# Performance work log

Hardware: AMD Instinct MI355X
Metric: run time of the kernel (lower is better)

Reference implementation:

```python
import jax, jax.numpy as jnp
import numpy as np

N_PED = 131072      # total pedestrians (batch)
SEG = 64            # pedestrians per segment (equal-size groups)
N_SEQ = N_PED // SEG
D_IN = 256          # enc_h_dim
D_OUT = 128         # mlp_dim


def setup_inputs() -> dict:
    key = jax.random.key(0)
    k1, k2 = jax.random.split(key, 2)
    h_states = jax.random.normal(k1, (N_PED, D_IN), dtype=jnp.float32)
    W = jax.random.normal(k2, (D_IN, D_OUT), dtype=jnp.float32) * 0.05
    b = jnp.zeros((D_OUT,), dtype=jnp.float32)
    starts = jnp.arange(N_SEQ, dtype=jnp.int64) * SEG
    seq_start_end = jnp.stack([starts, starts + SEG], axis=1)  # [N_SEQ, 2]
    return {"h_states": h_states, "W": W, "b": b, "seq_start_end": seq_start_end}


def reference(h_states, W, b, seq_start_end):
    # fc projection: (N, D_IN) -> (N, D_OUT)
    h = h_states @ W + b
    # gather each segment: equal-size groups of SEG pedestrians
    starts = seq_start_end[:, 0]                     # [G]
    idx = starts[:, None] + jnp.arange(SEG)[None, :]  # [G, S]
    seg = h[idx]                                      # [G, S, D_OUT]
    # per-segment self-attention pooling: softmax(H H^T) @ H
    scores = jnp.einsum('gsd,gtd->gst', seg, seg)     # [G, S, S]
    attn = jax.nn.softmax(scores, axis=-1)
    ctx = jnp.einsum('gst,gtd->gsd', attn, seg)       # [G, S, D_OUT]
    return ctx.reshape(-1, D_OUT)                     # [N, D_OUT]
```

## Files before the change

kernel.cpp:

```cpp
#include <hip/hip_runtime.h>
#include <stdint.h>

#define SEG 64
#define D_IN 256
#define D_OUT 128
#define NSEQ 2048

typedef __attribute__((ext_vector_type(8))) _Float16 half8;
typedef __attribute__((ext_vector_type(4))) float floatx4;

static __device__ __forceinline__ unsigned short f2h_bits(float f) {
  union { _Float16 h; unsigned short u; } v; v.h = (_Float16)f; return v.u;
}
static __device__ __forceinline__ unsigned pack2(float a, float b) {
  return (unsigned)f2h_bits(a) | ((unsigned)f2h_bits(b) << 16);
}

__global__ void prep_w_kernel(const float* __restrict__ W,
                              unsigned short* __restrict__ Wf) {
  const int idx = blockIdx.x * 256 + threadIdx.x;
  const float v = W[idx];
  const int k = idx >> 7, n = idx & 127;
  const int slot = (((n >> 4) * 8 + (k >> 5)) * 64 + ((n & 15) + 16 * ((k >> 3) & 3))) * 8 + (k & 7);
  Wf[slot] = f2h_bits(v);
}

struct SharedHT {
  union {
    unsigned short h[4][4][64][8];
    unsigned short pb[4][2][64][8];
  };
  unsigned short ht[8][2][64][8];
};
union alignas(16) SharedU {
  unsigned short a[4][8][64][8];
  SharedHT s;
};

__global__ __launch_bounds__(256, 4)
void attn_fused(const float* __restrict__ hs,
                const unsigned short* __restrict__ Wf,
                const float* __restrict__ bias,
                float* __restrict__ out)
{
  __shared__ SharedU u;

  const int g    = blockIdx.x;
  const int tid  = (int)threadIdx.x;
  const int w    = tid >> 6;
  const int lane = tid & 63;
  const int c    = lane & 15;
  const int q    = lane >> 4;

  {
    const float4* gsrc = (const float4*)(hs + (size_t)g * (SEG * D_IN));
#pragma unroll
    for (int i = 0; i < 4; ++i) {
      const int qb = i * 1024 + tid * 4;
      const float4 v0 = gsrc[qb + 0];
      const float4 v1 = gsrc[qb + 1];
      const float4 v2 = gsrc[qb + 2];
      const float4 v3 = gsrc[qb + 3];
      const int row  = i * 16 + (tid >> 4);
      const int ks   = (tid & 15) >> 1;
      const int slot = (row & 15) + ((tid & 1) << 5);
      unsigned short* d0 = &u.a[row >> 4][ks][slot][0];
      uint4 wa, wb;
      wa.x = pack2(v0.x, v0.y); wa.y = pack2(v0.z, v0.w);
      wa.z = pack2(v1.x, v1.y); wa.w = pack2(v1.z, v1.w);
      wb.x = pack2(v2.x, v2.y); wb.y = pack2(v2.z, v2.w);
      wb.z = pack2(v3.x, v3.y); wb.w = pack2(v3.z, v3.w);
      *(uint4*)d0         = wa;
      *(uint4*)(d0 + 128) = wb;
    }
  }

  const half8* WfV = (const half8*)Wf;
  const half8 wpre0 = WfV[((2 * w + 0) * 8 + 0) * 64 + lane];
  const half8 wpre1 = WfV[((2 * w + 1) * 8 + 0) * 64 + lane];

  float bv[2];
#pragma unroll
  for (int nt = 0; nt < 2; ++nt) bv[nt] = bias[(2 * w + nt) * 16 + c];
  floatx4 acc[2][4];
#pragma unroll
  for (int nt = 0; nt < 2; ++nt)
#pragma unroll
    for (int mt = 0; mt < 4; ++mt)
      acc[nt][mt] = (floatx4){bv[nt], bv[nt], bv[nt], bv[nt]};

  __syncthreads();

#pragma unroll
  for (int ks = 0; ks < 8; ++ks) {
    const half8 wf0 = ks ? WfV[((2 * w + 0) * 8 + ks) * 64 + lane] : wpre0;
    const half8 wf1 = ks ? WfV[((2 * w + 1) * 8 + ks) * 64 + lane] : wpre1;
    half8 af[4];
#pragma unroll
    for (int mt = 0; mt < 4; ++mt)
      af[mt] = *(const half8*)(&u.a[mt][ks][lane][0]);
#pragma unroll
    for (int mt = 0; mt < 4; ++mt) {
      acc[0][mt] = __builtin_amdgcn_mfma_f32_16x16x32_f16(af[mt], wf0, acc[0][mt], 0, 0, 0);
      acc[1][mt] = __builtin_amdgcn_mfma_f32_16x16x32_f16(af[mt], wf1, acc[1][mt], 0, 0, 0);
    }
  }

  __syncthreads();

#pragma unroll
  for (int nt = 0; nt < 2; ++nt) {
    const int ntg = 2 * w + nt;
#pragma unroll
    for (int mt = 0; mt < 4; ++mt) {
      unsigned short hb[4];
#pragma unroll
      for (int i = 0; i < 4; ++i) hb[i] = f2h_bits(acc[nt][mt][i]);
      const int lph = 16 * ((2 * nt + (c >> 3)) & 3);
#pragma unroll
      for (int i = 0; i < 4; ++i)
        u.s.h[mt][w][4 * q + i + lph][c & 7] = hb[i];
      const int lanep = c + 16 * ((2 * mt + (q >> 1)) & 3);
      const unsigned lo = (unsigned)hb[0] | ((unsigned)hb[1] << 16);
      const unsigned hi = (unsigned)hb[2] | ((unsigned)hb[3] << 16);
      *(uint2*)(&u.s.ht[ntg][mt >> 1][lanep][(q & 1) * 4]) = make_uint2(lo, hi);
    }
  }

  __syncthreads();

  floatx4 sacc[4];
#pragma unroll
  for (int nt = 0; nt < 4; ++nt) sacc[nt] = (floatx4){0.f, 0.f, 0.f, 0.f};
#pragma unroll
  for (int ks = 0; ks < 4; ++ks) {
    const half8 a = *(const half8*)(&u.s.h[w][ks][lane][0]);
#pragma unroll
    for (int nt = 0; nt < 4; ++nt) {
      const half8 b = *(const half8*)(&u.s.h[nt][ks][lane][0]);
      sacc[nt] = __builtin_amdgcn_mfma_f32_16x16x32_f16(a, b, sacc[nt], 0, 0, 0);
    }
  }

  float ev[4][4];
  float inv[4];
#pragma unroll
  for (int i = 0; i < 4; ++i) {
    float m = fmaxf(fmaxf(sacc[0][i], sacc[1][i]), fmaxf(sacc[2][i], sacc[3][i]));
#pragma unroll
    for (int d = 1; d < 16; d <<= 1) m = fmaxf(m, __shfl_xor(m, d, 64));
    float ssum = 0.f;
#pragma unroll
    for (int nt = 0; nt < 4; ++nt) {
      ev[i][nt] = __expf(sacc[nt][i] - m);
      ssum += ev[i][nt];
    }
#pragma unroll
    for (int d = 1; d < 16; d <<= 1) ssum += __shfl_xor(ssum, d, 64);
    inv[i] = 1.0f / ssum;
  }

  __syncthreads();

#pragma unroll
  for (int i = 0; i < 4; ++i)
#pragma unroll
    for (int nt = 0; nt < 4; ++nt)
      u.s.pb[w][nt >> 1][4 * q + i + 16 * ((2 * nt + (c >> 3)) & 3)][c & 7] =
          f2h_bits(ev[i][nt] * inv[i]);

  floatx4 cacc[8];
#pragma unroll
  for (int dt = 0; dt < 8; ++dt) cacc[dt] = (floatx4){0.f, 0.f, 0.f, 0.f};
#pragma unroll
  for (int kt = 0; kt < 2; ++kt) {
    const half8 pf = *(const half8*)(&u.s.pb[w][kt][lane][0]);
#pragma unroll
    for (int dt = 0; dt < 8; ++dt) {
      const half8 hf = *(const half8*)(&u.s.ht[dt][kt][lane][0]);
      cacc[dt] = __builtin_amdgcn_mfma_f32_16x16x32_f16(hf, pf, cacc[dt], 0, 0, 0);
    }
  }

  float* orow = out + ((size_t)g * SEG + 16 * w + c) * D_OUT + 4 * q;
#pragma unroll
  for (int dt = 0; dt < 8; ++dt)
    *(floatx4*)(orow + 16 * dt) = cacc[dt];
}

extern "C" void kernel_launch(void* const* d_in, const int* in_sizes, int n_in,
                              void* d_out, int out_size, void* d_ws, size_t ws_size,
                              hipStream_t stream) {
  const float* hs   = (const float*)d_in[0];
  const float* W    = (const float*)d_in[1];
  const float* bias = (const float*)d_in[2];
  float* out = (float*)d_out;
  unsigned short* Wf = (unsigned short*)d_ws;

  prep_w_kernel<<<128, 256, 0, stream>>>(W, Wf);
  attn_fused<<<NSEQ, 256, 0, stream>>>(hs, Wf, bias, out);
}
```

Measured before the change: 221.8 us.

## Make attention kernel persistent with register-staged prefetch of next segment

The grid shrinks from one block per segment to 512 persistent blocks, each looping over four segments. While the current segment's projection runs, the next segment's input is loaded into registers and written to a separate, no-longer-aliased shared buffer, so global-load latency overlaps with MFMA work. The cost is a larger shared footprint and heavy register use (16 float4 staging registers), and launch bounds drop to 2 blocks per CU, which lowers occupancy and may give less latency hiding than the original many-block launch.

New measurement: 222.7 us. About the same (+0.4%).

```diff
diff --git a/kernel.cpp b/kernel.cpp
--- a/kernel.cpp
+++ b/kernel.cpp
@@ -5,6 +5,7 @@
 #define D_IN 256
 #define D_OUT 128
 #define NSEQ 2048
+#define NBLK 512
 
 typedef __attribute__((ext_vector_type(8))) _Float16 half8;
 typedef __attribute__((ext_vector_type(4))) float floatx4;
@@ -32,28 +33,32 @@
   };
   unsigned short ht[8][2][64][8];
 };
-union alignas(16) SharedU {
+struct alignas(16) SharedAll {
   unsigned short a[4][8][64][8];
   SharedHT s;
 };
 
-__global__ __launch_bounds__(256, 4)
+__global__ __launch_bounds__(256, 2)
 void attn_fused(const float* __restrict__ hs,
                 const unsigned short* __restrict__ Wf,
                 const float* __restrict__ bias,
                 float* __restrict__ out)
 {
-  __shared__ SharedU u;
-
-  const int g    = blockIdx.x;
+  __shared__ SharedAll u;
+
+  const int bid  = blockIdx.x;
   const int tid  = (int)threadIdx.x;
   const int w    = tid >> 6;
   const int lane = tid & 63;
   const int c    = lane & 15;
   const int q    = lane >> 4;
 
+  const int srow  = tid >> 4;
+  const int sks   = (tid & 15) >> 1;
+  const int sslot = ((tid & 1) << 5);
+
   {
-    const float4* gsrc = (const float4*)(hs + (size_t)g * (SEG * D_IN));
+    const float4* gsrc = (const float4*)(hs + (size_t)bid * (SEG * D_IN));
 #pragma unroll
     for (int i = 0; i < 4; ++i) {
       const int qb = i * 1024 + tid * 4;
@@ -61,10 +66,8 @@
       const float4 v1 = gsrc[qb + 1];
       const float4 v2 = gsrc[qb + 2];
       const float4 v3 = gsrc[qb + 3];
-      const int row  = i * 16 + (tid >> 4);
-      const int ks   = (tid & 15) >> 1;
-      const int slot = (row & 15) + ((tid & 1) << 5);
-      unsigned short* d0 = &u.a[row >> 4][ks][slot][0];
+      const int row = i * 16 + srow;
+      unsigned short* d0 = &u.a[row >> 4][sks][(row & 15) + sslot][0];
       uint4 wa, wb;
       wa.x = pack2(v0.x, v0.y); wa.y = pack2(v0.z, v0.w);
       wa.z = pack2(v1.x, v1.y); wa.w = pack2(v1.z, v1.w);
@@ -75,117 +78,149 @@
     }
   }
 
+  float bv[2];
+#pragma unroll
+  for (int nt = 0; nt < 2; ++nt) bv[nt] = bias[(2 * w + nt) * 16 + c];
+
   const half8* WfV = (const half8*)Wf;
-  const half8 wpre0 = WfV[((2 * w + 0) * 8 + 0) * 64 + lane];
-  const half8 wpre1 = WfV[((2 * w + 1) * 8 + 0) * 64 + lane];
-
-  float bv[2];
-#pragma unroll
-  for (int nt = 0; nt < 2; ++nt) bv[nt] = bias[(2 * w + nt) * 16 + c];
-  floatx4 acc[2][4];
-#pragma unroll
-  for (int nt = 0; nt < 2; ++nt)
-#pragma unroll
-    for (int mt = 0; mt < 4; ++mt)
-      acc[nt][mt] = (floatx4){bv[nt], bv[nt], bv[nt], bv[nt]};
 
   __syncthreads();
 
-#pragma unroll
-  for (int ks = 0; ks < 8; ++ks) {
-    const half8 wf0 = ks ? WfV[((2 * w + 0) * 8 + ks) * 64 + lane] : wpre0;
-    const half8 wf1 = ks ? WfV[((2 * w + 1) * 8 + ks) * 64 + lane] : wpre1;
-    half8 af[4];
-#pragma unroll
-    for (int mt = 0; mt < 4; ++mt)
-      af[mt] = *(const half8*)(&u.a[mt][ks][lane][0]);
-#pragma unroll
-    for (int mt = 0; mt < 4; ++mt) {
-      acc[0][mt] = __builtin_amdgcn_mfma_f32_16x16x32_f16(af[mt], wf0, acc[0][mt], 0, 0, 0);
-      acc[1][mt] = __builtin_amdgcn_mfma_f32_16x16x32_f16(af[mt], wf1, acc[1][mt], 0, 0, 0);
-    }
+  for (int it = 0; it < 4; ++it) {
+    const int seg = bid + NBLK * it;
+
+    float4 st[16];
+    if (it < 3) {
+      const float4* gn = (const float4*)(hs + (size_t)(seg + NBLK) * (SEG * D_IN));
+#pragma unroll
+      for (int i = 0; i < 4; ++i)
+#pragma unroll
+        for (int k2 = 0; k2 < 4; ++k2)
+          st[4 * i + k2] = gn[i * 1024 + tid * 4 + k2];
+    }
+
+    floatx4 acc[2][4];
+#pragma unroll
+    for (int nt = 0; nt < 2; ++nt)
+#pragma unroll
+      for (int mt = 0; mt < 4; ++mt)
+        acc[nt][mt] = (floatx4){bv[nt], bv[nt], bv[nt], bv[nt]};
+
+#pragma unroll
+    for (int ks = 0; ks < 8; ++ks) {
+      const half8 wf0 = WfV[((2 * w + 0) * 8 + ks) * 64 + lane];
+      const half8 wf1 = WfV[((2 * w + 1) * 8 + ks) * 64 + lane];
+      half8 af[4];
+#pragma unroll
+      for (int mt = 0; mt < 4; ++mt)
+        af[mt] = *(const half8*)(&u.a[mt][ks][lane][0]);
+#pragma unroll
+      for (int mt = 0; mt < 4; ++mt) {
+        acc[0][mt] = __builtin_amdgcn_mfma_f32_16x16x32_f16(af[mt], wf0, acc[0][mt], 0, 0, 0);
+        acc[1][mt] = __builtin_amdgcn_mfma_f32_16x16x32_f16(af[mt], wf1, acc[1][mt], 0, 0, 0);
+      }
+    }
+
+    __syncthreads();
+
+    if (it < 3) {
+#pragma unroll
+      for (int i = 0; i < 4; ++i) {
+        const int row = i * 16 + srow;
+        unsigned short* d0 = &u.a[row >> 4][sks][(row & 15) + sslot][0];
+        uint4 wa, wb;
+        wa.x = pack2(st[4 * i + 0].x, st[4 * i + 0].y);
+        wa.y = pack2(st[4 * i + 0].z, st[4 * i + 0].w);
+        wa.z = pack2(st[4 * i + 1].x, st[4 * i + 1].y);
+        wa.w = pack2(st[4 * i + 1].z, st[4 * i + 1].w);
+        wb.x = pack2(st[4 * i + 2].x, st[4 * i + 2].y);
+        wb.y = pack2(st[4 * i + 2].z, st[4 * i + 2].w);
+        wb.z = pack2(st[4 * i + 3].x, st[4 * i + 3].y);
+        wb.w = pack2(st[4 * i + 3].z, st[4 * i + 3].w);
+        *(uint4*)d0         = wa;
+        *(uint4*)(d0 + 128) = wb;
+      }
+    }
+
+#pragma unroll
+    for (int nt = 0; nt < 2; ++nt) {
+      const int ntg = 2 * w + nt;
+#pragma unroll
+      for (int mt = 0; mt < 4; ++mt) {
+        unsigned short hb[4];
+#pragma unroll
+        for (int i = 0; i < 4; ++i) hb[i] = f2h_bits(acc[nt][mt][i]);
+        const int lph = 16 * ((2 * nt + (c >> 3)) & 3);
+#pragma unroll
+        for (int i = 0; i < 4; ++i)
+          u.s.h[mt][w][4 * q + i + lph][c & 7] = hb[i];
+        const int lanep = c + 16 * ((2 * mt + (q >> 1)) & 3);
+        const unsigned lo = (unsigned)hb[0] | ((unsigned)hb[1] << 16);
+        const unsigned hi = (unsigned)hb[2] | ((unsigned)hb[3] << 16);
+        *(uint2*)(&u.s.ht[ntg][mt >> 1][lanep][(q & 1) * 4]) = make_uint2(lo, hi);
+      }
+    }
+
+    __syncthreads();
+
+    floatx4 sacc[4];
+#pragma unroll
+    for (int nt = 0; nt < 4; ++nt) sacc[nt] = (floatx4){0.f, 0.f, 0.f, 0.f};
+#pragma unroll
+    for (int ks = 0; ks < 4; ++ks) {
+      const half8 a = *(const half8*)(&u.s.h[w][ks][lane][0]);
+#pragma unroll
+      for (int nt = 0; nt < 4; ++nt) {
+        const half8 b = *(const half8*)(&u.s.h[nt][ks][lane][0]);
+        sacc[nt] = __builtin_amdgcn_mfma_f32_16x16x32_f16(a, b, sacc[nt], 0, 0, 0);
+      }
+    }
+
+    float ev[4][4];
+    float inv[4];
+#pragma unroll
+    for (int i = 0; i < 4; ++i) {
+      float m = fmaxf(fmaxf(sacc[0][i], sacc[1][i]), fmaxf(sacc[2][i], sacc[3][i]));
+#pragma unroll
+      for (int d = 1; d < 16; d <<= 1) m = fmaxf(m, __shfl_xor(m, d, 64));
+      float ssum = 0.f;
+#pragma unroll
+      for (int nt = 0; nt < 4; ++nt) {
+        ev[i][nt] = __expf(sacc[nt][i] - m);
+        ssum += ev[i][nt];
+      }
+#pragma unroll
+      for (int d = 1; d < 16; d <<= 1) ssum += __shfl_xor(ssum, d, 64);
+      inv[i] = 1.0f / ssum;
+    }
+
+    __syncthreads();
+
+#pragma unroll
+    for (int i = 0; i < 4; ++i)
+#pragma unroll
+      for (int nt = 0; nt < 4; ++nt)
+        u.s.pb[w][nt >> 1][4 * q + i + 16 * ((2 * nt + (c >> 3)) & 3)][c & 7] =
+            f2h_bits(ev[i][nt] * inv[i]);
+
+    floatx4 cacc[8];
+#pragma unroll
+    for (int dt = 0; dt < 8; ++dt) cacc[dt] = (floatx4){0.f, 0.f, 0.f, 0.f};
+#pragma unroll
+    for (int kt = 0; kt < 2; ++kt) {
+      const half8 pf = *(const half8*)(&u.s.pb[w][kt][lane][0]);
+#pragma unroll
+      for (int dt = 0; dt < 8; ++dt) {
+        const half8 hf = *(const half8*)(&u.s.ht[dt][kt][lane][0]);
+        cacc[dt] = __builtin_amdgcn_mfma_f32_16x16x32_f16(hf, pf, cacc[dt], 0, 0, 0);
+      }
+    }
+
+    float* orow = out + ((size_t)seg * SEG + 16 * w + c) * D_OUT + 4 * q;
+#pragma unroll
+    for (int dt = 0; dt < 8; ++dt)
+      *(floatx4*)(orow + 16 * dt) = cacc[dt];
   }
-
-  __syncthreads();
-
-#pragma unroll
-  for (int nt = 0; nt < 2; ++nt) {
-    const int ntg = 2 * w + nt;
-#pragma unroll
-    for (int mt = 0; mt < 4; ++mt) {
-      unsigned short hb[4];
-#pragma unroll
-      for (int i = 0; i < 4; ++i) hb[i] = f2h_bits(acc[nt][mt][i]);
-      const int lph = 16 * ((2 * nt + (c >> 3)) & 3);
-#pragma unroll
-      for (int i = 0; i < 4; ++i)
-        u.s.h[mt][w][4 * q + i + lph][c & 7] = hb[i];
-      const int lanep = c + 16 * ((2 * mt + (q >> 1)) & 3);
-      const unsigned lo = (unsigned)hb[0] | ((unsigned)hb[1] << 16);
-      const unsigned hi = (unsigned)hb[2] | ((unsigned)hb[3] << 16);
-      *(uint2*)(&u.s.ht[ntg][mt >> 1][lanep][(q & 1) * 4]) = make_uint2(lo, hi);
-    }
-  }
-
-  __syncthreads();
-
-  floatx4 sacc[4];
-#pragma unroll
-  for (int nt = 0; nt < 4; ++nt) sacc[nt] = (floatx4){0.f, 0.f, 0.f, 0.f};
-#pragma unroll
-  for (int ks = 0; ks < 4; ++ks) {
-    const half8 a = *(const half8*)(&u.s.h[w][ks][lane][0]);
-#pragma unroll
-    for (int nt = 0; nt < 4; ++nt) {
-      const half8 b = *(const half8*)(&u.s.h[nt][ks][lane][0]);
-      sacc[nt] = __builtin_amdgcn_mfma_f32_16x16x32_f16(a, b, sacc[nt], 0, 0, 0);
-    }
-  }
-
-  float ev[4][4];
-  float inv[4];
-#pragma unroll
-  for (int i = 0; i < 4; ++i) {
-    float m = fmaxf(fmaxf(sacc[0][i], sacc[1][i]), fmaxf(sacc[2][i], sacc[3][i]));
-#pragma unroll
-    for (int d = 1; d < 16; d <<= 1) m = fmaxf(m, __shfl_xor(m, d, 64));
-    float ssum = 0.f;
-#pragma unroll
-    for (int nt = 0; nt < 4; ++nt) {
-      ev[i][nt] = __expf(sacc[nt][i] - m);
-      ssum += ev[i][nt];
-    }
-#pragma unroll
-    for (int d = 1; d < 16; d <<= 1) ssum += __shfl_xor(ssum, d, 64);
-    inv[i] = 1.0f / ssum;
-  }
-
-  __syncthreads();
-
-#pragma unroll
-  for (int i = 0; i < 4; ++i)
-#pragma unroll
-    for (int nt = 0; nt < 4; ++nt)
-      u.s.pb[w][nt >> 1][4 * q + i + 16 * ((2 * nt + (c >> 3)) & 3)][c & 7] =
-          f2h_bits(ev[i][nt] * inv[i]);
-
-  floatx4 cacc[8];
-#pragma unroll
-  for (int dt = 0; dt < 8; ++dt) cacc[dt] = (floatx4){0.f, 0.f, 0.f, 0.f};
-#pragma unroll
-  for (int kt = 0; kt < 2; ++kt) {
-    const half8 pf = *(const half8*)(&u.s.pb[w][kt][lane][0]);
-#pragma unroll
-    for (int dt = 0; dt < 8; ++dt) {
-      const half8 hf = *(const half8*)(&u.s.ht[dt][kt][lane][0]);
-      cacc[dt] = __builtin_amdgcn_mfma_f32_16x16x32_f16(hf, pf, cacc[dt], 0, 0, 0);
-    }
-  }
-
-  float* orow = out + ((size_t)g * SEG + 16 * w + c) * D_OUT + 4 * q;
-#pragma unroll
-  for (int dt = 0; dt < 8; ++dt)
-    *(floatx4*)(orow + 16 * dt) = cacc[dt];
 }
 
 extern "C" void kernel_launch(void* const* d_in, const int* in_sizes, int n_in,
@@ -198,5 +233,5 @@
   unsigned short* Wf = (unsigned short*)d_ws;
 
   prep_w_kernel<<<128, 256, 0, stream>>>(W, Wf);
-  attn_fused<<<NSEQ, 256, 0, stream>>>(hs, Wf, bias, out);
-}
+  attn_fused<<<NBLK, 256, 0, stream>>>(hs, Wf, bias, out);
+}
```
